# Kernel tuning notes

Measured on AMD Instinct MI355X. Metric: run time of the kernel, lower is better.

The kernel has to match this reference:

```python
import jax, jax.numpy as jnp
import numpy as np

NBLOCK = 2000
DIM = 2048
B, T = 32, 1024
EPS = 1e-12  # F.normalize eps


def _l2norm(v, axis):
    n = jnp.sqrt(jnp.sum(v * v, axis=axis, keepdims=True))
    return v / jnp.maximum(n, EPS)


def setup_inputs() -> dict:
    key = jax.random.key(0)
    kx, km, kw = jax.random.split(key, 3)
    x = jax.random.normal(kx, (B, T, DIM), dtype=jnp.float32)
    mask = jax.random.randint(km, (B, T), 0, 2).astype(jnp.int32)
    stdv = 1.0 / np.sqrt(DIM)
    weight = jax.random.uniform(kw, (NBLOCK, DIM), dtype=jnp.float32,
                                minval=-stdv, maxval=stdv)
    return {"x": x, "mask": mask, "weight": weight}


def reference(x, mask, weight):
    half = x.shape[0] // 2
    nblock = weight.shape[0]
    m = mask.astype(x.dtype)  # [B, T]

    # diversity: || W W^T - I ||_F
    gram = weight @ weight.T  # [N, N]
    diversity_loss = jnp.linalg.norm(gram - jnp.eye(nblock, dtype=weight.dtype))

    # cosine-similarity attention: [B, T, N]
    att = jnp.einsum('btd,nd->btn', _l2norm(x, axis=2), _l2norm(weight, axis=1))

    # uniformity loss: masked sum over T, softmax over blocks, mean over half-batch
    s = jnp.einsum('btn,bt->nb', att[:half], m[:half])  # [N, half]
    tmp = jnp.mean(jax.nn.softmax(s, axis=0), axis=1)   # [N]
    u_loss = jnp.linalg.norm(tmp)

    # per-row min over masked positions of the top-1 similarity
    top1 = jnp.max(att, axis=2)  # [B, T] (only topk[...,0] is used)
    inf = jnp.asarray(jnp.inf, dtype=x.dtype)
    masked_top1 = jnp.where(m > 0, top1, inf)
    min_sim = jnp.min(masked_top1[:half], axis=1)   # [half]
    ab_min = jnp.min(masked_top1[half:], axis=1)    # [half]

    return (0.2 * diversity_loss,
            2.0 - jnp.mean(min_sim) + jnp.mean(ab_min),
            0.5 * u_loss)
```

## Files before the change

### kernel.cpp

```cpp
#include <hip/hip_runtime.h>

typedef unsigned short u16;
typedef unsigned int u32;
typedef __attribute__((ext_vector_type(8))) short short8;
typedef __attribute__((ext_vector_type(8))) u16 ushort8;
typedef __attribute__((ext_vector_type(4))) u16 ushort4_t;
typedef __attribute__((ext_vector_type(4))) float fx4;

#define DIMK 2048
#define NBLK 2000

typedef const __attribute__((address_space(1))) void* gp_t;
typedef __attribute__((address_space(3))) void* lp_t;

__device__ __forceinline__ u16 f2bf(float f) {
  u32 u = __float_as_uint(f);
  u32 r = (u + 0x7fffu + ((u >> 16) & 1u)) >> 16;
  return (u16)r;
}

__device__ __forceinline__ u32 fkey(float f) {
  u32 u = __float_as_uint(f);
  return (u & 0x80000000u) ? ~u : (u | 0x80000000u);
}
__device__ __forceinline__ float dekey(u32 k) {
  u32 u = (k & 0x80000000u) ? (k ^ 0x80000000u) : ~k;
  return __uint_as_float(u);
}

__device__ __forceinline__ void gemm_tile(const u16* __restrict__ Abase,
                                          const u16* __restrict__ Bbase,
                                          int row0, int col0,
                                          u16* lsA, u16* lsB,
                                          fx4 acc[4][4])
{
  const int tid  = threadIdx.x;
  const int wv   = tid >> 6;
  const int lane = tid & 63;
  const int wr   = wv & 1, wc = wv >> 1;
  const int quad = lane >> 4, lc = lane & 15;

  const int srow = wv * 32 + (lane >> 2);
  const int skel = (((lane & 3) ^ ((lane >> 3) & 3)) * 8);
  const u16* gA0 = Abase + (size_t)(row0 + srow) * DIMK + skel;
  const u16* gA1 = gA0 + (size_t)16 * DIMK;
  const u16* gB0 = Bbase + (size_t)(col0 + srow) * DIMK + skel;
  const u16* gB1 = gB0 + (size_t)16 * DIMK;
  u16* lA0 = lsA + wv * 1024;
  u16* lA1 = lsA + wv * 1024 + 512;
  u16* lB0 = lsB + wv * 1024;
  u16* lB1 = lsB + wv * 1024 + 512;

  const int fIntra = lc * 32 + ((quad ^ ((lc >> 1) & 3)) * 8);

#pragma unroll
  for (int mi = 0; mi < 4; mi++)
#pragma unroll
    for (int ni = 0; ni < 4; ni++)
      acc[mi][ni] = fx4{0.f, 0.f, 0.f, 0.f};

  for (int k0 = 0; k0 < DIMK; k0 += 32) {
    __syncthreads();
    __builtin_amdgcn_global_load_lds((gp_t)gA0, (lp_t)lA0, 16, 0, 0);
    __builtin_amdgcn_global_load_lds((gp_t)gA1, (lp_t)lA1, 16, 0, 0);
    __builtin_amdgcn_global_load_lds((gp_t)gB0, (lp_t)lB0, 16, 0, 0);
    __builtin_amdgcn_global_load_lds((gp_t)gB1, (lp_t)lB1, 16, 0, 0);
    gA0 += 32; gA1 += 32; gB0 += 32; gB1 += 32;
    __syncthreads();
    short8 af[4], bfr[4];
#pragma unroll
    for (int mi = 0; mi < 4; mi++)
      af[mi] = *(const short8*)(lsA + (wr * 4 + mi) * 512 + fIntra);
#pragma unroll
    for (int ni = 0; ni < 4; ni++)
      bfr[ni] = *(const short8*)(lsB + (wc * 4 + ni) * 512 + fIntra);
#pragma unroll
    for (int mi = 0; mi < 4; mi++)
#pragma unroll
      for (int ni = 0; ni < 4; ni++)
        acc[mi][ni] = __builtin_amdgcn_mfma_f32_16x16x32_bf16(af[mi], bfr[ni], acc[mi][ni], 0, 0, 0);
  }
}

__global__ __launch_bounds__(256) void norm_rows_x(const float* __restrict__ x,
                                                   u16* __restrict__ Xn)
{
  const int wv = threadIdx.x >> 6, lane = threadIdx.x & 63;
  const int row = blockIdx.x * 4 + wv;
  const float4* xr = (const float4*)(x + (size_t)row * DIMK);
  float4 v[8];
  float ss = 0.f;
#pragma unroll
  for (int j = 0; j < 8; j++) {
    v[j] = xr[j * 64 + lane];
    ss += v[j].x*v[j].x + v[j].y*v[j].y + v[j].z*v[j].z + v[j].w*v[j].w;
  }
#pragma unroll
  for (int off = 1; off < 64; off <<= 1) ss += __shfl_xor(ss, off);
  float inv = 1.0f / fmaxf(sqrtf(ss), 1e-12f);
  ushort4_t* o = (ushort4_t*)(Xn + (size_t)row * DIMK);
#pragma unroll
  for (int j = 0; j < 8; j++) {
    ushort4_t t;
    t[0] = f2bf(v[j].x * inv); t[1] = f2bf(v[j].y * inv);
    t[2] = f2bf(v[j].z * inv); t[3] = f2bf(v[j].w * inv);
    o[j * 64 + lane] = t;
  }
}

__global__ __launch_bounds__(256) void norm_rows_w(const float* __restrict__ w,
                                                   u16* __restrict__ Wn,
                                                   u16* __restrict__ Wb)
{
  const int wv = threadIdx.x >> 6, lane = threadIdx.x & 63;
  const int row = blockIdx.x * 4 + wv;
  ushort4_t* on_ = (ushort4_t*)(Wn + (size_t)row * DIMK);
  ushort4_t* ob_ = (ushort4_t*)(Wb + (size_t)row * DIMK);
  if (row < NBLK) {
    const float4* wr_ = (const float4*)(w + (size_t)row * DIMK);
    float4 v[8];
    float ss = 0.f;
#pragma unroll
    for (int j = 0; j < 8; j++) {
      v[j] = wr_[j * 64 + lane];
      ss += v[j].x*v[j].x + v[j].y*v[j].y + v[j].z*v[j].z + v[j].w*v[j].w;
    }
#pragma unroll
    for (int off = 1; off < 64; off <<= 1) ss += __shfl_xor(ss, off);
    float inv = 1.0f / fmaxf(sqrtf(ss), 1e-12f);
#pragma unroll
    for (int j = 0; j < 8; j++) {
      ushort4_t tn, tb;
      tn[0] = f2bf(v[j].x * inv); tn[1] = f2bf(v[j].y * inv);
      tn[2] = f2bf(v[j].z * inv); tn[3] = f2bf(v[j].w * inv);
      tb[0] = f2bf(v[j].x); tb[1] = f2bf(v[j].y);
      tb[2] = f2bf(v[j].z); tb[3] = f2bf(v[j].w);
      on_[j * 64 + lane] = tn;
      ob_[j * 64 + lane] = tb;
    }
  } else {
    ushort4_t z = ushort4_t{0, 0, 0, 0};
#pragma unroll
    for (int j = 0; j < 8; j++) { on_[j * 64 + lane] = z; ob_[j * 64 + lane] = z; }
  }
}

__global__ __launch_bounds__(256) void gram_kernel(const u16* __restrict__ Wb,
                                                   float* __restrict__ divsum)
{
  __shared__ __align__(16) u16 lsA[4096];
  __shared__ __align__(16) u16 lsB[4096];
  fx4 acc[4][4];
  const int i0 = blockIdx.y * 128, j0 = blockIdx.x * 128;
  gemm_tile(Wb, Wb, i0, j0, lsA, lsB, acc);
  const int tid = threadIdx.x, wv = tid >> 6, lane = tid & 63;
  const int wr = wv & 1, wc = wv >> 1, quad = lane >> 4, lc = lane & 15;
  float local = 0.f;
#pragma unroll
  for (int mi = 0; mi < 4; mi++) {
#pragma unroll
    for (int ni = 0; ni < 4; ni++) {
#pragma unroll
      for (int r = 0; r < 4; r++) {
        int i = i0 + wr * 64 + mi * 16 + quad * 4 + r;
        int j = j0 + wc * 64 + ni * 16 + lc;
        float g = acc[mi][ni][r];
        float d = (i == j && i < NBLK) ? 1.0f : 0.0f;
        float e = g - d;
        local += e * e;
      }
    }
  }
#pragma unroll
  for (int off = 1; off < 64; off <<= 1) local += __shfl_xor(local, off);
  if (lane == 0) atomicAdd(divsum, local);
}

__global__ __launch_bounds__(256) void att_kernel(const u16* __restrict__ Xn,
                                                  const u16* __restrict__ Wn,
                                                  const int* __restrict__ mask,
                                                  u32* __restrict__ top1k,
                                                  float* __restrict__ s)
{
  __shared__ __align__(16) u16 lsA[4096];
  __shared__ __align__(16) u16 lsB[4096];
  __shared__ float sMask[128];
  const int xb = blockIdx.x, yb = blockIdx.y;
  const int tid = threadIdx.x;
  if (tid < 128) sMask[tid] = (float)mask[yb * 128 + tid];
  fx4 acc[4][4];
  gemm_tile(Xn, Wn, yb * 128, xb * 128, lsA, lsB, acc);
  const int wv = tid >> 6, lane = tid & 63;
  const int wr = wv & 1, wc = wv >> 1, quad = lane >> 4, lc = lane & 15;
  const int colbase = xb * 128 + wc * 64;

#pragma unroll
  for (int mi = 0; mi < 4; mi++) {
#pragma unroll
    for (int r = 0; r < 4; r++) {
      float v = -3.0e38f;
#pragma unroll
      for (int ni = 0; ni < 4; ni++) {
        int col = colbase + ni * 16 + lc;
        float av = acc[mi][ni][r];
        v = (col < NBLK && av > v) ? av : v;
      }
      v = fmaxf(v, __shfl_xor(v, 1));
      v = fmaxf(v, __shfl_xor(v, 2));
      v = fmaxf(v, __shfl_xor(v, 4));
      v = fmaxf(v, __shfl_xor(v, 8));
      if (lc == 0) {
        int row = yb * 128 + wr * 64 + mi * 16 + quad * 4 + r;
        atomicMax(&top1k[row], fkey(v));
      }
    }
  }

  if (yb < 128) {
    const int b = yb >> 3;
#pragma unroll
    for (int ni = 0; ni < 4; ni++) {
      float sv = 0.f;
#pragma unroll
      for (int mi = 0; mi < 4; mi++) {
#pragma unroll
        for (int r = 0; r < 4; r++)
          sv += sMask[wr * 64 + mi * 16 + quad * 4 + r] * acc[mi][ni][r];
      }
      sv += __shfl_xor(sv, 16);
      sv += __shfl_xor(sv, 32);
      int col = colbase + ni * 16 + lc;
      if (quad == 0 && col < NBLK)
        atomicAdd(&s[b * 2048 + col], sv);
    }
  }
}

__global__ __launch_bounds__(256) void softmax_kernel(const float* __restrict__ s,
                                                      float* __restrict__ tmp)
{
  const int b = blockIdx.x, tid = threadIdx.x;
  const float* sb = s + b * 2048;
  __shared__ float red[4];
  float mx = -3.0e38f;
  for (int n = tid; n < NBLK; n += 256) mx = fmaxf(mx, sb[n]);
#pragma unroll
  for (int off = 1; off < 64; off <<= 1) mx = fmaxf(mx, __shfl_xor(mx, off));
  if ((tid & 63) == 0) red[tid >> 6] = mx;
  __syncthreads();
  mx = fmaxf(fmaxf(red[0], red[1]), fmaxf(red[2], red[3]));
  __syncthreads();
  float se = 0.f;
  for (int n = tid; n < NBLK; n += 256) se += expf(sb[n] - mx);
#pragma unroll
  for (int off = 1; off < 64; off <<= 1) se += __shfl_xor(se, off);
  if ((tid & 63) == 0) red[tid >> 6] = se;
  __syncthreads();
  se = red[0] + red[1] + red[2] + red[3];
  float scale = 1.0f / (se * 16.0f);
  for (int n = tid; n < NBLK; n += 256) atomicAdd(&tmp[n], expf(sb[n] - mx) * scale);
}

__global__ __launch_bounds__(1024) void finalize_kernel(const u32* __restrict__ top1k,
                                                        const int* __restrict__ mask,
                                                        const float* __restrict__ tmp,
                                                        const float* __restrict__ divsum,
                                                        float* __restrict__ out)
{
  const int tid = threadIdx.x;
  __shared__ float sMin[32];
  __shared__ float sSq[16];
  const int b = tid >> 5, li = tid & 31;
  float mn = 3.0e38f;
  for (int t = li; t < 1024; t += 32) {
    int idx = b * 1024 + t;
    if (mask[idx] > 0) mn = fminf(mn, dekey(top1k[idx]));
  }
#pragma unroll
  for (int off = 1; off < 32; off <<= 1) mn = fminf(mn, __shfl_xor(mn, off));
  if (li == 0) sMin[b] = mn;
  float ssq = 0.f;
  for (int n = tid; n < NBLK; n += 1024) { float v = tmp[n]; ssq += v * v; }
#pragma unroll
  for (int off = 1; off < 64; off <<= 1) ssq += __shfl_xor(ssq, off);
  if ((tid & 63) == 0) sSq[tid >> 6] = ssq;
  __syncthreads();
  if (tid == 0) {
    float m0 = 0.f, m1 = 0.f;
    for (int i = 0; i < 16; i++) { m0 += sMin[i]; m1 += sMin[16 + i]; }
    m0 *= (1.0f / 16.0f); m1 *= (1.0f / 16.0f);
    float sq = 0.f;
    for (int i = 0; i < 16; i++) sq += sSq[i];
    out[0] = 0.2f * sqrtf(divsum[0]);
    out[1] = 2.0f - m0 + m1;
    out[2] = 0.5f * sqrtf(sq);
  }
}

extern "C" void kernel_launch(void* const* d_in, const int* in_sizes, int n_in,
                              void* d_out, int out_size, void* d_ws, size_t ws_size,
                              hipStream_t stream) {
  const float* x    = (const float*)d_in[0];
  const int*   mask = (const int*)d_in[1];
  const float* w    = (const float*)d_in[2];
  float* out = (float*)d_out;

  char* ws = (char*)d_ws;
  u32*   top1k  = (u32*)(ws);
  float* s      = (float*)(ws + 131072);
  float* tmp    = (float*)(ws + 262144);
  float* divsum = (float*)(ws + 270336);
  u16*   Xn     = (u16*)(ws + 270592);
  u16*   Wn     = (u16*)(ws + 270592 + 134217728ull);
  u16*   Wb     = (u16*)(ws + 270592 + 134217728ull + 8388608ull);

  hipMemsetAsync(ws, 0, 270592, stream);

  norm_rows_w<<<dim3(512), dim3(256), 0, stream>>>(w, Wn, Wb);
  norm_rows_x<<<dim3(8192), dim3(256), 0, stream>>>(x, Xn);
  gram_kernel<<<dim3(16, 16), dim3(256), 0, stream>>>(Wb, divsum);
  att_kernel<<<dim3(16, 256), dim3(256), 0, stream>>>(Xn, Wn, mask, top1k, s);
  softmax_kernel<<<dim3(16), dim3(256), 0, stream>>>(s, tmp);
  finalize_kernel<<<dim3(1), dim3(1024), 0, stream>>>(top1k, mask, tmp, divsum, out);
}
```

Measured before the change: 791.3 us.

## Rewrite attention GEMM with 256x256 tiles and 4-stage async LDS ring pipeline

The attention GEMM moves from 128x128 tiles with 256 threads (via gemm_tile) to 256x256 tiles with 512 threads. Operands stream through a 4-slot LDS ring using global_load_lds direct loads with swizzled addressing and vmcnt-based waits, so loads overlap MFMA work. Work-group IDs are remapped so neighbouring blocks share row panels, which should improve L2 reuse. It also raises MFMA setprio during compute. The larger tiles cut global traffic per FLOP, at the cost of more register pressure and 128KB of LDS per block.

```diff
diff --git a/kernel.cpp b/kernel.cpp
--- a/kernel.cpp
+++ b/kernel.cpp
@@ -176,32 +176,94 @@
   if (lane == 0) atomicAdd(divsum, local);
 }
 
-__global__ __launch_bounds__(256) void att_kernel(const u16* __restrict__ Xn,
-                                                  const u16* __restrict__ Wn,
-                                                  const int* __restrict__ mask,
-                                                  u32* __restrict__ top1k,
-                                                  float* __restrict__ s)
-{
-  __shared__ __align__(16) u16 lsA[4096];
-  __shared__ __align__(16) u16 lsB[4096];
-  __shared__ float sMask[128];
-  const int xb = blockIdx.x, yb = blockIdx.y;
-  const int tid = threadIdx.x;
-  if (tid < 128) sMask[tid] = (float)mask[yb * 128 + tid];
-  fx4 acc[4][4];
-  gemm_tile(Xn, Wn, yb * 128, xb * 128, lsA, lsB, acc);
-  const int wv = tid >> 6, lane = tid & 63;
-  const int wr = wv & 1, wc = wv >> 1, quad = lane >> 4, lc = lane & 15;
-  const int colbase = xb * 128 + wc * 64;
-
-#pragma unroll
-  for (int mi = 0; mi < 4; mi++) {
+__global__ __launch_bounds__(512, 2) void att_kernel(const u16* __restrict__ Xn,
+                                                     const u16* __restrict__ Wn,
+                                                     const int* __restrict__ mask,
+                                                     u32* __restrict__ top1k,
+                                                     float* __restrict__ s)
+{
+  __shared__ __align__(16) u16 ring[4][2][8192];
+
+  const int orig = blockIdx.x;
+  const int wg   = ((orig & 7) << 7) | (orig >> 3);
+  const int xb   = wg & 7;
+  const int yb   = wg >> 3;
+  const int row0 = yb << 8, col0 = xb << 8;
+
+  const int tid  = threadIdx.x;
+  const int wv   = tid >> 6, lane = tid & 63;
+  const int wr   = wv >> 2, wc = wv & 3;
+  const int quad = lane >> 4, lc = lane & 15;
+
+  const int srow = wv * 32 + (lane >> 2);
+  const int skel = (((lane & 3) ^ ((lane >> 3) & 3)) << 3);
+  const u16* gA0 = Xn + (size_t)(row0 + srow) * DIMK + skel;
+  const u16* gA1 = gA0 + (size_t)16 * DIMK;
+  const u16* gB0 = Wn + (size_t)(col0 + srow) * DIMK + skel;
+  const u16* gB1 = gB0 + (size_t)16 * DIMK;
+
+  const int fIntra = lc * 32 + ((quad ^ ((lc >> 1) & 3)) << 3);
+
+  fx4 acc[8][4];
+#pragma unroll
+  for (int mi = 0; mi < 8; mi++)
+#pragma unroll
+    for (int ni = 0; ni < 4; ni++)
+      acc[mi][ni] = fx4{0.f, 0.f, 0.f, 0.f};
+
+#define STAGE(slot, kt)                                                          \
+  do {                                                                           \
+    const int ko_ = (kt) << 5;                                                   \
+    u16* lA_ = &ring[(slot)][0][wv << 10];                                       \
+    u16* lB_ = &ring[(slot)][1][wv << 10];                                       \
+    __builtin_amdgcn_global_load_lds((gp_t)(gA0 + ko_), (lp_t)lA_,         16, 0, 0); \
+    __builtin_amdgcn_global_load_lds((gp_t)(gA1 + ko_), (lp_t)(lA_ + 512), 16, 0, 0); \
+    __builtin_amdgcn_global_load_lds((gp_t)(gB0 + ko_), (lp_t)lB_,         16, 0, 0); \
+    __builtin_amdgcn_global_load_lds((gp_t)(gB1 + ko_), (lp_t)(lB_ + 512), 16, 0, 0); \
+  } while (0)
+
+  STAGE(0, 0);
+  STAGE(1, 1);
+  STAGE(2, 2);
+
+  const int NT = DIMK / 32;
+  for (int t = 0; t < NT; ++t) {
+    if (t <= NT - 3)      asm volatile("s_waitcnt vmcnt(8)" ::: "memory");
+    else if (t == NT - 2) asm volatile("s_waitcnt vmcnt(4)" ::: "memory");
+    else                  asm volatile("s_waitcnt vmcnt(0)" ::: "memory");
+    __builtin_amdgcn_s_barrier();
+    __builtin_amdgcn_sched_barrier(0);
+
+    if (t + 3 < NT) STAGE((t + 3) & 3, t + 3);
+
+    const u16* lAt = &ring[t & 3][0][0];
+    const u16* lBt = &ring[t & 3][1][0];
+    short8 af[8], bfr[4];
+#pragma unroll
+    for (int mi = 0; mi < 8; mi++)
+      af[mi] = *(const short8*)(lAt + (wr * 8 + mi) * 512 + fIntra);
+#pragma unroll
+    for (int ni = 0; ni < 4; ni++)
+      bfr[ni] = *(const short8*)(lBt + (wc * 4 + ni) * 512 + fIntra);
+
+    __builtin_amdgcn_s_setprio(1);
+#pragma unroll
+    for (int mi = 0; mi < 8; mi++)
+#pragma unroll
+      for (int ni = 0; ni < 4; ni++)
+        acc[mi][ni] = __builtin_amdgcn_mfma_f32_16x16x32_bf16(af[mi], bfr[ni], acc[mi][ni], 0, 0, 0);
+    __builtin_amdgcn_s_setprio(0);
+  }
+#undef STAGE
+
+#pragma unroll
+  for (int mi = 0; mi < 8; mi++) {
 #pragma unroll
     for (int r = 0; r < 4; r++) {
       float v = -3.0e38f;
 #pragma unroll
       for (int ni = 0; ni < 4; ni++) {
-        int col = colbase + ni * 16 + lc;
+        int col = col0 + wc * 64 + ni * 16 + lc;
         float av = acc[mi][ni][r];
         v = (col < NBLK && av > v) ? av : v;
       }
@@ -210,28 +272,33 @@
       v = fmaxf(v, __shfl_xor(v, 4));
       v = fmaxf(v, __shfl_xor(v, 8));
       if (lc == 0) {
-        int row = yb * 128 + wr * 64 + mi * 16 + quad * 4 + r;
+        int row = row0 + wr * 128 + mi * 16 + quad * 4 + r;
         atomicMax(&top1k[row], fkey(v));
       }
     }
   }
 
-  if (yb < 128) {
-    const int b = yb >> 3;
+  if (yb < 64) {
+    const int b = yb >> 2;
+    float sv[4] = {0.f, 0.f, 0.f, 0.f};
+#pragma unroll
+    for (int mi = 0; mi < 8; mi++) {
+#pragma unroll
+      for (int r = 0; r < 4; r++) {
+        float mval = (float)mask[row0 + wr * 128 + mi * 16 + quad * 4 + r];
+#pragma unroll
+        for (int ni = 0; ni < 4; ni++)
+          sv[ni] += mval * acc[mi][ni][r];
+      }
+    }
 #pragma unroll
     for (int ni = 0; ni < 4; ni++) {
-      float sv = 0.f;
-#pragma unroll
-      for (int mi = 0; mi < 4; mi++) {
-#pragma unroll
-        for (int r = 0; r < 4; r++)
-          sv += sMask[wr * 64 + mi * 16 + quad * 4 + r] * acc[mi][ni][r];
-      }
-      sv += __shfl_xor(sv, 16);
-      sv += __shfl_xor(sv, 32);
-      int col = colbase + ni * 16 + lc;
+      float v = sv[ni];
+      v += __shfl_xor(v, 16);
+      v += __shfl_xor(v, 32);
+      int col = col0 + wc * 64 + ni * 16 + lc;
       if (quad == 0 && col < NBLK)
-        atomicAdd(&s[b * 2048 + col], sv);
+        atomicAdd(&s[b * 2048 + col], v);
     }
   }
 }
@@ -319,7 +386,7 @@
   norm_rows_w<<<dim3(512), dim3(256), 0, stream>>>(w, Wn, Wb);
   norm_rows_x<<<dim3(8192), dim3(256), 0, stream>>>(x, Xn);
   gram_kernel<<<dim3(16, 16), dim3(256), 0, stream>>>(Wb, divsum);
-  att_kernel<<<dim3(16, 256), dim3(256), 0, stream>>>(Xn, Wn, mask, top1k, s);
+  att_kernel<<<dim3(1024), dim3(512), 0, stream>>>(Xn, Wn, mask, top1k, s);
   softmax_kernel<<<dim3(16), dim3(256), 0, stream>>>(s, tmp);
   finalize_kernel<<<dim3(1), dim3(1024), 0, stream>>>(top1k, mask, tmp, divsum, out);
 }
```

New measurement: 730.3 us. 7.7% less time.
